# Performance work log

Measured on AMD Instinct MI355X. Metric: run time of the kernel, lower is better.

Reference implementation:

```python
import jax, jax.numpy as jnp
import numpy as np

N_WIRES = 6
DIM = 1 << N_WIRES  # 64, equals input channel dim C for amplitude encoding
HID = N_WIRES       # hidden_dim = len(ops)


def _rx(theta):
    c = jnp.cos(theta / 2).astype(jnp.complex64)
    s = jnp.sin(theta / 2).astype(jnp.complex64)
    return jnp.stack([jnp.stack([c, -1j * s]), jnp.stack([-1j * s, c])])


def _ry(theta):
    c = jnp.cos(theta / 2).astype(jnp.complex64)
    s = jnp.sin(theta / 2).astype(jnp.complex64)
    return jnp.stack([jnp.stack([c, -s]), jnp.stack([s, c])])


def _apply_1q(state, U, wire):
    # state: (N, 2, 2, ..., 2); apply 2x2 U on qubit axis wire+1
    s = jnp.moveaxis(state, wire + 1, 1)
    s = jnp.einsum('ab,nb...->na...', U, s)
    return jnp.moveaxis(s, 1, wire + 1)


def _apply_cnot(state, c, t):
    # flip target axis where control bit == 1
    s = jnp.moveaxis(state, (c + 1, t + 1), (1, 2))
    s = jnp.concatenate([s[:, :1], jnp.flip(s[:, 1:2], axis=2)], axis=1)
    return jnp.moveaxis(s, (1, 2), (c + 1, t + 1))


def _expval_z(state, wire):
    # <Z_wire> = P(bit=0) - P(bit=1)
    p = state.real ** 2 + state.imag ** 2
    p = jnp.moveaxis(p, wire + 1, 1).reshape(p.shape[0], 2, -1)
    return p[:, 0].sum(-1) - p[:, 1].sum(-1)


def _value_layer(x_flat, params, qk):
    # amplitude encoding: normalize input into state amplitudes (C == DIM)
    norm = jnp.linalg.norm(x_flat, axis=-1, keepdims=True)
    psi = (x_flat / norm).astype(jnp.complex64)
    state = psi.reshape((x_flat.shape[0],) + (2,) * N_WIRES)
    rx0, ry0, ry1 = params[0], params[1], params[2]
    for j in range(N_WIRES):
        state = _apply_1q(state, _rx(rx0[j]), j)
        state = _apply_1q(state, _ry(ry0[j]), j)
    for j in range(N_WIRES):
        state = _apply_cnot(state, j, (j + 1) % N_WIRES)
    for j in range(N_WIRES):
        state = _apply_1q(state, _ry(ry1[j]), j)
    if qk:
        z0 = _expval_z(state, 0)
        return jnp.stack([z0] * HID, axis=-1)  # qk=True replicates wire-0 <Z>
    return jnp.stack([_expval_z(state, w) for w in range(N_WIRES)], axis=-1)


def setup_inputs() -> dict:
    key = jax.random.key(0)
    k1, k2, k3, k4 = jax.random.split(key, 4)
    B, T, C = 16, 2048, DIM
    return {
        'x': jax.random.normal(k1, (B, T, C), dtype=jnp.float32),
        'params_q': jax.random.normal(k2, (3, N_WIRES), dtype=jnp.float32),
        'params_k': jax.random.normal(k3, (3, N_WIRES), dtype=jnp.float32),
        'params_v': jax.random.normal(k4, (3, N_WIRES), dtype=jnp.float32),
    }


def reference(x, params_q, params_k, params_v):
    B, T, C = x.shape
    xf = x.reshape(B * T, C)
    q = _value_layer(xf, params_q, True).reshape(B, T, HID)
    k = _value_layer(xf, params_k, True).reshape(B, T, HID)
    v = _value_layer(xf, params_v, False).reshape(B, T, HID)
    scores = jnp.einsum('btd,bsd->bts', q, k) / jnp.sqrt(jnp.float32(HID))
    attn = jax.nn.softmax(scores, axis=-1)
    return jnp.einsum('bts,bsd->btd', attn, v)
```

## Files before the change

### kernel.cpp

```cpp
#include <hip/hip_runtime.h>
#include <math.h>

#define NWIRES 6
#define DIM 64
#define NTOK 32768
#define NBATCH 16
#define TPB 2048
#define NMOM 16
#define SQRT6F 2.4494897427831781f
#define APAD 72

typedef short bf16x8 __attribute__((ext_vector_type(8)));
typedef float f32x4  __attribute__((ext_vector_type(4)));

__device__ __forceinline__ unsigned f2bfbits(float f) {
    unsigned u = __float_as_uint(f);
    return (u + 0x7FFF + ((u >> 16) & 1)) >> 16;
}
__device__ __forceinline__ float bfbits2f(unsigned b) {
    return __uint_as_float(b << 16);
}

template<int M>
__device__ __forceinline__ void ryr(float* v, float c, float s) {
#pragma unroll
    for (int i = 0; i < DIM; ++i) {
        if (i & M) continue;
        int j = i | M;
        float a = v[i], b = v[j];
        v[i] = c * a - s * b;
        v[j] = s * a + c * b;
    }
}
template<int MC, int MT>
__device__ __forceinline__ void cnr(float* v) {
#pragma unroll
    for (int i = 0; i < DIM; ++i) {
        if (!(i & MC) || (i & MT)) continue;
        int j = i | MT;
        float t = v[i]; v[i] = v[j]; v[j] = t;
    }
}

__global__ __attribute__((amdgpu_waves_per_eu(1, 1)))
__launch_bounds__(64) void qsa_prepA(const float* __restrict__ pq,
                                     const float* __restrict__ pk,
                                     const float* __restrict__ pv,
                                     unsigned short* __restrict__ Apack) {
    int c = blockIdx.x, ph = blockIdx.y;
    int k = threadIdx.x;
    __shared__ float sT[64];
    __shared__ float sP[24];
    const float* p = (c == 0) ? pq : (c == 1 ? pk : pv);
    float d = 0.f;
#pragma unroll
    for (int j = 0; j < 6; ++j)
        d += 0.5f * p[j] * ((k & (32 >> j)) ? -1.f : 1.f);
    float sd, cd;
    sincosf(d, &sd, &cd);
    sT[k] = ph ? sd : cd;
    if (k < 12) {
        float s, cc;
        sincosf(0.5f * p[6 + k], &s, &cc);
        sP[k * 2 + 0] = cc;
        sP[k * 2 + 1] = s;
    }
    __syncthreads();

    float v[DIM];
#pragma unroll
    for (int i = 0; i < DIM; ++i)
        v[i] = (__popc(i & k) & 1) ? -sT[i] : sT[i];
#pragma unroll
    for (int M = 32; M >= 1; M >>= 1) {
#pragma unroll
        for (int i = 0; i < DIM; ++i) {
            if (i & M) continue;
            int j = i | M;
            float a = v[i], b = v[j];
            v[i] = a + b; v[j] = a - b;
        }
    }
    ryr<32>(v, sP[0],  sP[1]);
    ryr<16>(v, sP[2],  sP[3]);
    ryr< 8>(v, sP[4],  sP[5]);
    ryr< 4>(v, sP[6],  sP[7]);
    ryr< 2>(v, sP[8],  sP[9]);
    ryr< 1>(v, sP[10], sP[11]);
    cnr<32,16>(v); cnr<16,8>(v); cnr<8,4>(v);
    cnr<4,2>(v);   cnr<2,1>(v);  cnr<1,32>(v);
    ryr<32>(v, sP[12], sP[13]);
    ryr<16>(v, sP[14], sP[15]);
    ryr< 8>(v, sP[16], sP[17]);
    ryr< 4>(v, sP[18], sP[19]);
    ryr< 2>(v, sP[20], sP[21]);
    ryr< 1>(v, sP[22], sP[23]);

    unsigned short* Ah = Apack + (size_t)c * 16384;
    unsigned short* Al = Ah + 8192;
#pragma unroll
    for (int r = 0; r < DIM; ++r) {
        unsigned hb = f2bfbits(v[r]);
        unsigned lb = f2bfbits(v[r] - bfbits2f(hb));
        int row = ph * 64 + r;
        Ah[row * 64 + k] = (unsigned short)hb;
        Al[row * 64 + k] = (unsigned short)lb;
    }
}

__global__ __launch_bounds__(256, 4) void qsa_sim(
        const float* __restrict__ x,
        const unsigned short* __restrict__ Apack,
        float* __restrict__ zq,
        float* __restrict__ kv) {
    __shared__ unsigned short sAh[128 * APAD];
    __shared__ unsigned short sAl[128 * APAD];
    int tid = threadIdx.x;
    int tbase = blockIdx.x * 64;
    int circ = blockIdx.y;

    const uint4* Agh = (const uint4*)(Apack + (size_t)circ * 16384);
    const uint4* Agl = (const uint4*)(Apack + (size_t)circ * 16384 + 8192);
#pragma unroll
    for (int it = 0; it < 4; ++it) {
        int i = it * 256 + tid;
        int r = i >> 3, ch = i & 7;
        *(uint4*)(&sAh[r * APAD + ch * 8]) = Agh[i];
        *(uint4*)(&sAl[r * APAD + ch * 8]) = Agl[i];
    }

    int lane = tid & 63, wv = tid >> 6;
    int q4 = lane >> 4, c16 = lane & 15;
    int mytok = wv * 16 + c16;
    const float* xr = x + ((size_t)(tbase + mytok)) * 64;
    bf16x8 xh[2], xl[2];
#pragma unroll
    for (int ks = 0; ks < 2; ++ks) {
        float4 f0 = *(const float4*)(xr + ks * 32 + q4 * 8);
        float4 f1 = *(const float4*)(xr + ks * 32 + q4 * 8 + 4);
        float ff[8] = {f0.x, f0.y, f0.z, f0.w, f1.x, f1.y, f1.z, f1.w};
#pragma unroll
        for (int e = 0; e < 8; ++e) {
            unsigned hb = f2bfbits(ff[e]);
            unsigned lb = f2bfbits(ff[e] - bfbits2f(hb));
            xh[ks][e] = (short)hb;
            xl[ks][e] = (short)lb;
        }
    }
    __syncthreads();

    f32x4 acc[8];
#pragma unroll
    for (int mt = 0; mt < 8; ++mt) acc[mt] = (f32x4){0.f, 0.f, 0.f, 0.f};

#pragma unroll
    for (int mt = 0; mt < 8; ++mt) {
        int r = mt * 16 + c16;
#pragma unroll
        for (int ks = 0; ks < 2; ++ks) {
            bf16x8 ah = *(const bf16x8*)(&sAh[r * APAD + ks * 32 + q4 * 8]);
            bf16x8 al = *(const bf16x8*)(&sAl[r * APAD + ks * 32 + q4 * 8]);
            acc[mt] = __builtin_amdgcn_mfma_f32_16x16x32_bf16(ah, xh[ks], acc[mt], 0, 0, 0);
            acc[mt] = __builtin_amdgcn_mfma_f32_16x16x32_bf16(ah, xl[ks], acc[mt], 0, 0, 0);
            acc[mt] = __builtin_amdgcn_mfma_f32_16x16x32_bf16(al, xh[ks], acc[mt], 0, 0, 0);
        }
    }

    float n = 0.f, s0 = 0.f, s1 = 0.f, s2 = 0.f, s3 = 0.f, s4 = 0.f, s5 = 0.f;
    float f2 = (q4 < 2) ? 1.f : 0.f;
    float f3 = (q4 & 1) ? 0.f : 1.f;
#pragma unroll
    for (int mt = 0; mt < 4; ++mt) {
#pragma unroll
        for (int rg = 0; rg < 4; ++rg) {
            float dc = acc[mt][rg];
            float ds = acc[mt + 4][rg];
            float p = dc * dc + ds * ds;
            n += p;
            if (!(mt & 2)) s0 += p;
            if (!(mt & 1)) s1 += p;
            s2 += f2 * p;
            s3 += f3 * p;
            if (!(rg & 2)) s4 += p;
            if (!(rg & 1)) s5 += p;
        }
    }
#pragma unroll
    for (int d = 16; d <= 32; d <<= 1) {
        n  += __shfl_xor(n,  d, 64);
        s0 += __shfl_xor(s0, d, 64);
        s1 += __shfl_xor(s1, d, 64);
        s2 += __shfl_xor(s2, d, 64);
        s3 += __shfl_xor(s3, d, 64);
        s4 += __shfl_xor(s4, d, 64);
        s5 += __shfl_xor(s5, d, 64);
    }
    if (q4 == 0) {
        int t = tbase + mytok;
        float inv = 1.0f / n;
        if (circ == 0) {
            zq[t] = SQRT6F * (2.f * s0 - n) * inv;
        } else if (circ == 1) {
            kv[(size_t)t * 8] = (2.f * s0 - n) * inv;
        } else {
            float* o = kv + (size_t)t * 8;
            o[1] = (2.f*s0 - n) * inv;
            o[2] = (2.f*s1 - n) * inv;
            o[3] = (2.f*s2 - n) * inv;
            o[4] = (2.f*s3 - n) * inv;
            o[5] = (2.f*s4 - n) * inv;
            o[6] = (2.f*s5 - n) * inv;
            o[7] = 0.f;
        }
    }
}

__global__ __attribute__((amdgpu_waves_per_eu(1, 2)))
__launch_bounds__(64) void qsa_moments_partial(
        const float* __restrict__ kv,
        float* __restrict__ mpart) {
    int blk = blockIdx.x;
    int b = blk >> 3, c = blk & 7;
    int lane = threadIdx.x;
    float S[NMOM], H[NMOM][6];
#pragma unroll
    for (int m = 0; m < NMOM; ++m) {
        S[m] = 0.f;
#pragma unroll
        for (int w = 0; w < 6; ++w) H[m][w] = 0.f;
    }
    const float* base = kv + ((size_t)(b * TPB + c * 256)) * 8;
#pragma unroll
    for (int r = 0; r < 4; ++r) {
        const float4* e = (const float4*)(base + (size_t)(r * 64 + lane) * 8);
        float4 e0 = e[0], e1 = e[1];
        float z = e0.x;
        float v0 = e0.y, v1 = e0.z, v2 = e0.w, v3 = e1.x, v4 = e1.y, v5 = e1.z;
        float pw = 1.f;
#pragma unroll
        for (int m = 0; m < NMOM; ++m) {
            S[m] += pw;
            H[m][0] += pw * v0; H[m][1] += pw * v1; H[m][2] += pw * v2;
            H[m][3] += pw * v3; H[m][4] += pw * v4; H[m][5] += pw * v5;
            pw *= z;
        }
    }
#pragma unroll
    for (int d = 32; d >= 1; d >>= 1) {
#pragma unroll
        for (int m = 0; m < NMOM; ++m) {
            S[m] += __shfl_xor(S[m], d, 64);
#pragma unroll
            for (int w = 0; w < 6; ++w) H[m][w] += __shfl_xor(H[m][w], d, 64);
        }
    }
    if (lane == 0) {
        float* o = mpart + (size_t)blk * 112;
#pragma unroll
        for (int m = 0; m < NMOM; ++m) {
            float* om = o + m * 7;
            om[0] = S[m];
            om[1] = H[m][0]; om[2] = H[m][1]; om[3] = H[m][2];
            om[4] = H[m][3]; om[5] = H[m][4]; om[6] = H[m][5];
        }
    }
}

__global__ __launch_bounds__(256) void qsa_eval(
        const float* __restrict__ zq,
        const float* __restrict__ mpart,
        float* __restrict__ out) {
    __shared__ float sm[112];
    int bk = blockIdx.x;
    int b = bk >> 3;
    int tid = threadIdx.x;
    if (tid < 112) {
        float s = 0.f;
#pragma unroll
        for (int c = 0; c < 8; ++c) s += mpart[(size_t)(b * 8 + c) * 112 + tid];
        sm[tid] = s;
    }
    __syncthreads();

    int t = bk * 256 + tid;
    float a = zq[t];
    float den = 0.f, o0 = 0.f, o1 = 0.f, o2 = 0.f, o3 = 0.f, o4 = 0.f, o5 = 0.f;
    float pw = 1.f;
#pragma unroll
    for (int m = 0; m < NMOM; ++m) {
        const float* mm = sm + m * 7;
        den += pw * mm[0];
        o0 += pw * mm[1]; o1 += pw * mm[2]; o2 += pw * mm[3];
        o3 += pw * mm[4]; o4 += pw * mm[5]; o5 += pw * mm[6];
        pw *= a * (1.0f / (m + 1));
    }
    float inv = 1.0f / den;
    float* o = out + (size_t)t * 6;
    float2* o2p = (float2*)o;
    o2p[0] = make_float2(o0 * inv, o1 * inv);
    o2p[1] = make_float2(o2 * inv, o3 * inv);
    o2p[2] = make_float2(o4 * inv, o5 * inv);
}

extern "C" void kernel_launch(void* const* d_in, const int* in_sizes, int n_in,
                              void* d_out, int out_size, void* d_ws, size_t ws_size,
                              hipStream_t stream) {
    const float* x  = (const float*)d_in[0];
    const float* pq = (const float*)d_in[1];
    const float* pk = (const float*)d_in[2];
    const float* pv = (const float*)d_in[3];
    float* w = (float*)d_ws;
    unsigned short* Apk  = (unsigned short*)w;
    float* zq            = w + 24576;
    float* kv            = zq + NTOK;
    float* mpart         = kv + NTOK * 8;
    float* out           = (float*)d_out;

    qsa_prepA<<<dim3(3, 2), 64, 0, stream>>>(pq, pk, pv, Apk);
    qsa_sim<<<dim3(NTOK / 64, 3), 256, 0, stream>>>(x, Apk, zq, kv);
    qsa_moments_partial<<<NBATCH * 8, 64, 0, stream>>>(kv, mpart);
    qsa_eval<<<NTOK / 256, 256, 0, stream>>>(zq, mpart, out);
}
```

Baseline: 87.13 us.

## Fuse circuit-matrix construction into sim kernel and process four token groups per block

Drops the separate prepA launch: each sim block now rebuilds the bf16 hi/lo circuit matrices in shared memory, splitting each column's 64-element transform across lane pairs with xor-shuffles. Each block now covers 256 tokens over a serial four-step loop, prefetching the next group's x rows while the current group's MFMAs run, so the in-block matrix build is amortised over more tokens. The LDS row pad changes from 72 to 76 and A fragments are read as two 8-byte loads. The trade-off is redundant trig and butterfly work in every block, a quarter as many blocks, and more register pressure from the prefetch buffers.

```diff
diff --git a/kernel.cpp b/kernel.cpp
--- a/kernel.cpp
+++ b/kernel.cpp
@@ -8,7 +8,7 @@
 #define TPB 2048
 #define NMOM 16
 #define SQRT6F 2.4494897427831781f
-#define APAD 72
+#define APAD 76
 
 typedef short bf16x8 __attribute__((ext_vector_type(8)));
 typedef float f32x4  __attribute__((ext_vector_type(4)));
@@ -20,197 +20,227 @@
 __device__ __forceinline__ float bfbits2f(unsigned b) {
     return __uint_as_float(b << 16);
 }
-
-template<int M>
-__device__ __forceinline__ void ryr(float* v, float c, float s) {
-#pragma unroll
-    for (int i = 0; i < DIM; ++i) {
-        if (i & M) continue;
-        int j = i | M;
-        float a = v[i], b = v[j];
-        v[i] = c * a - s * b;
-        v[j] = s * a + c * b;
-    }
-}
-template<int MC, int MT>
-__device__ __forceinline__ void cnr(float* v) {
-#pragma unroll
-    for (int i = 0; i < DIM; ++i) {
-        if (!(i & MC) || (i & MT)) continue;
-        int j = i | MT;
-        float t = v[i]; v[i] = v[j]; v[j] = t;
-    }
-}
-
-__global__ __attribute__((amdgpu_waves_per_eu(1, 1)))
-__launch_bounds__(64) void qsa_prepA(const float* __restrict__ pq,
-                                     const float* __restrict__ pk,
-                                     const float* __restrict__ pv,
-                                     unsigned short* __restrict__ Apack) {
-    int c = blockIdx.x, ph = blockIdx.y;
-    int k = threadIdx.x;
-    __shared__ float sT[64];
-    __shared__ float sP[24];
-    const float* p = (c == 0) ? pq : (c == 1 ? pk : pv);
-    float d = 0.f;
-#pragma unroll
-    for (int j = 0; j < 6; ++j)
-        d += 0.5f * p[j] * ((k & (32 >> j)) ? -1.f : 1.f);
-    float sd, cd;
-    sincosf(d, &sd, &cd);
-    sT[k] = ph ? sd : cd;
-    if (k < 12) {
-        float s, cc;
-        sincosf(0.5f * p[6 + k], &s, &cc);
-        sP[k * 2 + 0] = cc;
-        sP[k * 2 + 1] = s;
-    }
-    __syncthreads();
-
-    float v[DIM];
-#pragma unroll
-    for (int i = 0; i < DIM; ++i)
-        v[i] = (__popc(i & k) & 1) ? -sT[i] : sT[i];
-#pragma unroll
-    for (int M = 32; M >= 1; M >>= 1) {
-#pragma unroll
-        for (int i = 0; i < DIM; ++i) {
-            if (i & M) continue;
-            int j = i | M;
-            float a = v[i], b = v[j];
-            v[i] = a + b; v[j] = a - b;
-        }
-    }
-    ryr<32>(v, sP[0],  sP[1]);
-    ryr<16>(v, sP[2],  sP[3]);
-    ryr< 8>(v, sP[4],  sP[5]);
-    ryr< 4>(v, sP[6],  sP[7]);
-    ryr< 2>(v, sP[8],  sP[9]);
-    ryr< 1>(v, sP[10], sP[11]);
-    cnr<32,16>(v); cnr<16,8>(v); cnr<8,4>(v);
-    cnr<4,2>(v);   cnr<2,1>(v);  cnr<1,32>(v);
-    ryr<32>(v, sP[12], sP[13]);
-    ryr<16>(v, sP[14], sP[15]);
-    ryr< 8>(v, sP[16], sP[17]);
-    ryr< 4>(v, sP[18], sP[19]);
-    ryr< 2>(v, sP[20], sP[21]);
-    ryr< 1>(v, sP[22], sP[23]);
-
-    unsigned short* Ah = Apack + (size_t)c * 16384;
-    unsigned short* Al = Ah + 8192;
-#pragma unroll
-    for (int r = 0; r < DIM; ++r) {
-        unsigned hb = f2bfbits(v[r]);
-        unsigned lb = f2bfbits(v[r] - bfbits2f(hb));
-        int row = ph * 64 + r;
-        Ah[row * 64 + k] = (unsigned short)hb;
-        Al[row * 64 + k] = (unsigned short)lb;
-    }
-}
+__device__ __forceinline__ float pswap(float v) { return __shfl_xor(v, 1, 64); }
 
 __global__ __launch_bounds__(256, 4) void qsa_sim(
         const float* __restrict__ x,
-        const unsigned short* __restrict__ Apack,
+        const float* __restrict__ pq,
+        const float* __restrict__ pk,
+        const float* __restrict__ pv,
         float* __restrict__ zq,
         float* __restrict__ kv) {
     __shared__ unsigned short sAh[128 * APAD];
     __shared__ unsigned short sAl[128 * APAD];
+    __shared__ float sTc[64], sTs[64], sP[24];
     int tid = threadIdx.x;
-    int tbase = blockIdx.x * 64;
+    int tbase = blockIdx.x * 256;
     int circ = blockIdx.y;
-
-    const uint4* Agh = (const uint4*)(Apack + (size_t)circ * 16384);
-    const uint4* Agl = (const uint4*)(Apack + (size_t)circ * 16384 + 8192);
-#pragma unroll
-    for (int it = 0; it < 4; ++it) {
-        int i = it * 256 + tid;
-        int r = i >> 3, ch = i & 7;
-        *(uint4*)(&sAh[r * APAD + ch * 8]) = Agh[i];
-        *(uint4*)(&sAl[r * APAD + ch * 8]) = Agl[i];
-    }
+    const float* p = (circ == 0) ? pq : (circ == 1 ? pk : pv);
 
     int lane = tid & 63, wv = tid >> 6;
     int q4 = lane >> 4, c16 = lane & 15;
-    int mytok = wv * 16 + c16;
-    const float* xr = x + ((size_t)(tbase + mytok)) * 64;
+    int mytok0 = wv * 64 + 0 * 16 + c16;
+    const float* xr0 = x + ((size_t)(tbase + mytok0)) * 64;
+    float4 rw[4];
+#pragma unroll
+    for (int ks = 0; ks < 2; ++ks) {
+        rw[ks * 2 + 0] = *(const float4*)(xr0 + ks * 32 + q4 * 8);
+        rw[ks * 2 + 1] = *(const float4*)(xr0 + ks * 32 + q4 * 8 + 4);
+    }
+
+    if (tid < 64) {
+        int b = tid;
+        float d = 0.f;
+#pragma unroll
+        for (int j = 0; j < 6; ++j)
+            d += 0.5f * p[j] * ((b & (32 >> j)) ? -1.f : 1.f);
+        float sd, cd;
+        sincosf(d, &sd, &cd);
+        sTc[b] = cd;
+        sTs[b] = sd;
+        if (b < 12) {
+            float s, cc;
+            sincosf(0.5f * p[6 + b], &s, &cc);
+            sP[b * 2 + 0] = cc;
+            sP[b * 2 + 1] = s;
+        }
+    }
+    __syncthreads();
+
+    {
+        int ph = tid >> 7;
+        int k  = (tid >> 1) & 63;
+        int h  = tid & 1;
+        const float* sTx = ph ? sTs : sTc;
+        float v[32];
+#pragma unroll
+        for (int i = 0; i < 32; ++i) {
+            int g = h * 32 + i;
+            v[i] = (__popc(g & k) & 1) ? -sTx[g] : sTx[g];
+        }
+#pragma unroll
+        for (int i = 0; i < 32; ++i) {
+            float pv_ = pswap(v[i]);
+            v[i] = h ? (pv_ - v[i]) : (v[i] + pv_);
+        }
+#pragma unroll
+        for (int M = 16; M >= 1; M >>= 1) {
+#pragma unroll
+            for (int i = 0; i < 32; ++i) {
+                if (i & M) continue;
+                int j = i | M;
+                float a = v[i], b = v[j];
+                v[i] = a + b; v[j] = a - b;
+            }
+        }
+#pragma unroll
+        for (int layer = 0; layer < 2; ++layer) {
+            const float* Pl = sP + layer * 12;
+            {
+                float c = Pl[0], ss = h ? Pl[1] : -Pl[1];
+#pragma unroll
+                for (int i = 0; i < 32; ++i) {
+                    float pv_ = pswap(v[i]);
+                    v[i] = c * v[i] + ss * pv_;
+                }
+            }
+#pragma unroll
+            for (int w = 1; w < 6; ++w) {
+                int M = 32 >> w;
+                float c = Pl[w * 2], s = Pl[w * 2 + 1];
+#pragma unroll
+                for (int i = 0; i < 32; ++i) {
+                    if (i & M) continue;
+                    int j = i | M;
+                    float a = v[i], b = v[j];
+                    v[i] = c * a - s * b;
+                    v[j] = s * a + c * b;
+                }
+            }
+            if (layer == 0) {
+#pragma unroll
+                for (int i = 0; i < 16; ++i) {
+                    int j = i | 16;
+                    float a = v[i], b = v[j];
+                    v[i] = h ? b : a;
+                    v[j] = h ? a : b;
+                }
+#pragma unroll
+                for (int w = 1; w < 5; ++w) {
+                    int MC = 32 >> w, MT = MC >> 1;
+#pragma unroll
+                    for (int i = 0; i < 32; ++i) {
+                        if (!(i & MC) || (i & MT)) continue;
+                        int j = i | MT;
+                        float t = v[i]; v[i] = v[j]; v[j] = t;
+                    }
+                }
+#pragma unroll
+                for (int i = 1; i < 32; i += 2) v[i] = pswap(v[i]);
+            }
+        }
+#pragma unroll
+        for (int i = 0; i < 32; ++i) {
+            int row = ph * 64 + h * 32 + i;
+            unsigned hb = f2bfbits(v[i]);
+            unsigned lb = f2bfbits(v[i] - bfbits2f(hb));
+            sAh[row * APAD + k] = (unsigned short)hb;
+            sAl[row * APAD + k] = (unsigned short)lb;
+        }
+    }
+    __syncthreads();
+
     bf16x8 xh[2], xl[2];
-#pragma unroll
-    for (int ks = 0; ks < 2; ++ks) {
-        float4 f0 = *(const float4*)(xr + ks * 32 + q4 * 8);
-        float4 f1 = *(const float4*)(xr + ks * 32 + q4 * 8 + 4);
-        float ff[8] = {f0.x, f0.y, f0.z, f0.w, f1.x, f1.y, f1.z, f1.w};
-#pragma unroll
-        for (int e = 0; e < 8; ++e) {
-            unsigned hb = f2bfbits(ff[e]);
-            unsigned lb = f2bfbits(ff[e] - bfbits2f(hb));
-            xh[ks][e] = (short)hb;
-            xl[ks][e] = (short)lb;
-        }
-    }
-    __syncthreads();
-
-    f32x4 acc[8];
-#pragma unroll
-    for (int mt = 0; mt < 8; ++mt) acc[mt] = (f32x4){0.f, 0.f, 0.f, 0.f};
-
-#pragma unroll
-    for (int mt = 0; mt < 8; ++mt) {
-        int r = mt * 16 + c16;
+#pragma unroll 1
+    for (int cg = 0; cg < 4; ++cg) {
 #pragma unroll
         for (int ks = 0; ks < 2; ++ks) {
-            bf16x8 ah = *(const bf16x8*)(&sAh[r * APAD + ks * 32 + q4 * 8]);
-            bf16x8 al = *(const bf16x8*)(&sAl[r * APAD + ks * 32 + q4 * 8]);
-            acc[mt] = __builtin_amdgcn_mfma_f32_16x16x32_bf16(ah, xh[ks], acc[mt], 0, 0, 0);
-            acc[mt] = __builtin_amdgcn_mfma_f32_16x16x32_bf16(ah, xl[ks], acc[mt], 0, 0, 0);
-            acc[mt] = __builtin_amdgcn_mfma_f32_16x16x32_bf16(al, xh[ks], acc[mt], 0, 0, 0);
-        }
-    }
-
-    float n = 0.f, s0 = 0.f, s1 = 0.f, s2 = 0.f, s3 = 0.f, s4 = 0.f, s5 = 0.f;
-    float f2 = (q4 < 2) ? 1.f : 0.f;
-    float f3 = (q4 & 1) ? 0.f : 1.f;
-#pragma unroll
-    for (int mt = 0; mt < 4; ++mt) {
-#pragma unroll
-        for (int rg = 0; rg < 4; ++rg) {
-            float dc = acc[mt][rg];
-            float ds = acc[mt + 4][rg];
-            float p = dc * dc + ds * ds;
-            n += p;
-            if (!(mt & 2)) s0 += p;
-            if (!(mt & 1)) s1 += p;
-            s2 += f2 * p;
-            s3 += f3 * p;
-            if (!(rg & 2)) s4 += p;
-            if (!(rg & 1)) s5 += p;
-        }
-    }
-#pragma unroll
-    for (int d = 16; d <= 32; d <<= 1) {
-        n  += __shfl_xor(n,  d, 64);
-        s0 += __shfl_xor(s0, d, 64);
-        s1 += __shfl_xor(s1, d, 64);
-        s2 += __shfl_xor(s2, d, 64);
-        s3 += __shfl_xor(s3, d, 64);
-        s4 += __shfl_xor(s4, d, 64);
-        s5 += __shfl_xor(s5, d, 64);
-    }
-    if (q4 == 0) {
-        int t = tbase + mytok;
-        float inv = 1.0f / n;
-        if (circ == 0) {
-            zq[t] = SQRT6F * (2.f * s0 - n) * inv;
-        } else if (circ == 1) {
-            kv[(size_t)t * 8] = (2.f * s0 - n) * inv;
-        } else {
-            float* o = kv + (size_t)t * 8;
-            o[1] = (2.f*s0 - n) * inv;
-            o[2] = (2.f*s1 - n) * inv;
-            o[3] = (2.f*s2 - n) * inv;
-            o[4] = (2.f*s3 - n) * inv;
-            o[5] = (2.f*s4 - n) * inv;
-            o[6] = (2.f*s5 - n) * inv;
-            o[7] = 0.f;
+            float4 f0 = rw[ks * 2], f1 = rw[ks * 2 + 1];
+            float ff[8] = {f0.x, f0.y, f0.z, f0.w, f1.x, f1.y, f1.z, f1.w};
+#pragma unroll
+            for (int e = 0; e < 8; ++e) {
+                unsigned hb = f2bfbits(ff[e]);
+                unsigned lb = f2bfbits(ff[e] - bfbits2f(hb));
+                xh[ks][e] = (short)hb;
+                xl[ks][e] = (short)lb;
+            }
+        }
+        int mytok = wv * 64 + cg * 16 + c16;
+        if (cg < 3) {
+            const float* xrn = x + ((size_t)(tbase + mytok + 16)) * 64;
+#pragma unroll
+            for (int ks = 0; ks < 2; ++ks) {
+                rw[ks * 2 + 0] = *(const float4*)(xrn + ks * 32 + q4 * 8);
+                rw[ks * 2 + 1] = *(const float4*)(xrn + ks * 32 + q4 * 8 + 4);
+            }
+        }
+
+        f32x4 acc[8];
+#pragma unroll
+        for (int mt = 0; mt < 8; ++mt) acc[mt] = (f32x4){0.f, 0.f, 0.f, 0.f};
+#pragma unroll
+        for (int mt = 0; mt < 8; ++mt) {
+            int r = mt * 16 + c16;
+#pragma unroll
+            for (int ks = 0; ks < 2; ++ks) {
+                const uint2* ph_ = (const uint2*)(&sAh[r * APAD + ks * 32 + q4 * 8]);
+                const uint2* pl_ = (const uint2*)(&sAl[r * APAD + ks * 32 + q4 * 8]);
+                union { uint2 u[2]; bf16x8 v; } ua, ub;
+                ua.u[0] = ph_[0]; ua.u[1] = ph_[1];
+                ub.u[0] = pl_[0]; ub.u[1] = pl_[1];
+                bf16x8 ah = ua.v, al = ub.v;
+                acc[mt] = __builtin_amdgcn_mfma_f32_16x16x32_bf16(ah, xh[ks], acc[mt], 0, 0, 0);
+                acc[mt] = __builtin_amdgcn_mfma_f32_16x16x32_bf16(ah, xl[ks], acc[mt], 0, 0, 0);
+                acc[mt] = __builtin_amdgcn_mfma_f32_16x16x32_bf16(al, xh[ks], acc[mt], 0, 0, 0);
+            }
+        }
+
+        float n = 0.f, s0 = 0.f, s1 = 0.f, s2 = 0.f, s3 = 0.f, s4 = 0.f, s5 = 0.f;
+        float f2 = (q4 < 2) ? 1.f : 0.f;
+        float f3 = (q4 & 1) ? 0.f : 1.f;
+#pragma unroll
+        for (int mt = 0; mt < 4; ++mt) {
+#pragma unroll
+            for (int rg = 0; rg < 4; ++rg) {
+                float dc = acc[mt][rg];
+                float ds = acc[mt + 4][rg];
+                float pp = dc * dc + ds * ds;
+                n += pp;
+                if (!(mt & 2)) s0 += pp;
+                if (!(mt & 1)) s1 += pp;
+                s2 += f2 * pp;
+                s3 += f3 * pp;
+                if (!(rg & 2)) s4 += pp;
+                if (!(rg & 1)) s5 += pp;
+            }
+        }
+#pragma unroll
+        for (int d = 16; d <= 32; d <<= 1) {
+            n  += __shfl_xor(n,  d, 64);
+            s0 += __shfl_xor(s0, d, 64);
+            s1 += __shfl_xor(s1, d, 64);
+            s2 += __shfl_xor(s2, d, 64);
+            s3 += __shfl_xor(s3, d, 64);
+            s4 += __shfl_xor(s4, d, 64);
+            s5 += __shfl_xor(s5, d, 64);
+        }
+        if (q4 == 0) {
+            int t = tbase + mytok;
+            float inv = 1.0f / n;
+            if (circ == 0) {
+                zq[t] = SQRT6F * (2.f * s0 - n) * inv;
+            } else if (circ == 1) {
+                kv[(size_t)t * 8] = (2.f * s0 - n) * inv;
+            } else {
+                float* o = kv + (size_t)t * 8;
+                o[1] = (2.f*s0 - n) * inv;
+                o[2] = (2.f*s1 - n) * inv;
+                o[3] = (2.f*s2 - n) * inv;
+                o[4] = (2.f*s3 - n) * inv;
+                o[5] = (2.f*s4 - n) * inv;
+                o[6] = (2.f*s5 - n) * inv;
+                o[7] = 0.f;
+            }
         }
     }
 }
@@ -310,14 +340,12 @@
     const float* pk = (const float*)d_in[2];
     const float* pv = (const float*)d_in[3];
     float* w = (float*)d_ws;
-    unsigned short* Apk  = (unsigned short*)w;
-    float* zq            = w + 24576;
-    float* kv            = zq + NTOK;
-    float* mpart         = kv + NTOK * 8;
-    float* out           = (float*)d_out;
-
-    qsa_prepA<<<dim3(3, 2), 64, 0, stream>>>(pq, pk, pv, Apk);
-    qsa_sim<<<dim3(NTOK / 64, 3), 256, 0, stream>>>(x, Apk, zq, kv);
+    float* zq    = w;
+    float* kv    = zq + NTOK;
+    float* mpart = kv + NTOK * 8;
+    float* out   = (float*)d_out;
+
+    qsa_sim<<<dim3(NTOK / 256, 3), 256, 0, stream>>>(x, pq, pk, pv, zq, kv);
     qsa_moments_partial<<<NBATCH * 8, 64, 0, stream>>>(kv, mpart);
     qsa_eval<<<NTOK / 256, 256, 0, stream>>>(zq, mpart, out);
 }
```

Result: slower. 109.5 us (+25.6%).
